# Performance work log

Measured on AMD Instinct MI355X. Metric: run time of the kernel, lower is better.

## Reference

```python
import jax, jax.numpy as jnp
import numpy as np

N, IN_CH, HID, HEADS, NCLS, E = 50000, 128, 32, 8, 16, 800000
NEG_SLOPE = 0.2  # PyG GATConv default negative_slope


def setup_inputs() -> dict:
    key = jax.random.key(0)
    ks = jax.random.split(key, 10)
    sc = lambda fan: 1.0 / np.sqrt(fan).astype(np.float32)
    x = jax.random.normal(ks[0], (N, IN_CH), jnp.float32)
    edge_index = jax.random.randint(ks[1], (2, E), 0, N, jnp.int32)
    W1 = jax.random.normal(ks[2], (IN_CH, HEADS * HID), jnp.float32) * sc(IN_CH)
    att_src1 = jax.random.normal(ks[3], (HEADS, HID), jnp.float32) * sc(HID)
    att_dst1 = jax.random.normal(ks[4], (HEADS, HID), jnp.float32) * sc(HID)
    b1 = jnp.zeros((HEADS * HID,), jnp.float32)
    W2 = jax.random.normal(ks[5], (HEADS * HID, NCLS), jnp.float32) * sc(HEADS * HID)
    att_src2 = jax.random.normal(ks[6], (1, NCLS), jnp.float32) * sc(NCLS)
    att_dst2 = jax.random.normal(ks[7], (1, NCLS), jnp.float32) * sc(NCLS)
    b2 = jnp.zeros((NCLS,), jnp.float32)
    return {"x": x, "edge_index": edge_index, "W1": W1, "att_src1": att_src1,
            "att_dst1": att_dst1, "b1": b1, "W2": W2, "att_src2": att_src2,
            "att_dst2": att_dst2, "b2": b2}


def _gat_layer(x, W, a_src, a_dst, src, dst, heads, ch):
    """PyG GATConv core: per-edge LeakyReLU attention, scatter-softmax over
    destination neighborhoods, scatter-add aggregation. Returns [N, heads, ch]."""
    n = x.shape[0]
    h = (x @ W).reshape(n, heads, ch)                      # [N,H,C]
    e_src = jnp.einsum('nhc,hc->nh', h, a_src)             # [N,H]
    e_dst = jnp.einsum('nhc,hc->nh', h, a_dst)             # [N,H]
    e = jax.nn.leaky_relu(e_src[src] + e_dst[dst], NEG_SLOPE)  # [Etot,H]
    # scatter-softmax grouped by destination node (self-loops ensure nonempty)
    m = jax.ops.segment_max(e, dst, num_segments=n)        # [N,H]
    p = jnp.exp(e - m[dst])
    denom = jax.ops.segment_sum(p, dst, num_segments=n)    # [N,H]
    alpha = p / denom[dst]                                 # [Etot,H]
    out = jax.ops.segment_sum(alpha[:, :, None] * h[src], dst, num_segments=n)
    return out                                             # [N,H,C]


def reference(x, edge_index, W1, att_src1, att_dst1, b1, W2, att_src2, att_dst2, b2):
    n = x.shape[0]
    loops = jnp.arange(n, dtype=edge_index.dtype)          # add_self_loops=True
    src = jnp.concatenate([edge_index[0], loops])
    dst = jnp.concatenate([edge_index[1], loops])
    # conv1: heads=8, concat=True
    h1 = _gat_layer(x, W1, att_src1, att_dst1, src, dst, HEADS, HID)
    h1 = h1.reshape(n, HEADS * HID) + b1
    h1 = jax.nn.elu(h1)  # dropout is identity in eval mode
    # conv2: heads=1, concat=False (mean over 1 head == that head)
    h2 = _gat_layer(h1, W2, att_src2, att_dst2, src, dst, 1, NCLS)
    return h2[:, 0, :] + b2
```

## Files before the change

kernel.cpp:

```cpp
#include <hip/hip_runtime.h>
#include <hip/hip_bf16.h>


#define IN_CH 128
#define HIDC  256
#define NCLS  16
#define NEG_SLOPE 0.2f

typedef short bf16x8 __attribute__((ext_vector_type(8)));
typedef float f32x4 __attribute__((ext_vector_type(4)));

__device__ __forceinline__ unsigned int f2bf(float f) {
    unsigned int u = __float_as_uint(f);
    return (u + 0x7fffu + ((u >> 16) & 1u)) >> 16;
}
__device__ __forceinline__ float bf_lo(unsigned int w) { return __uint_as_float(w << 16); }
__device__ __forceinline__ float bf_hi(unsigned int w) { return __uint_as_float(w & 0xffff0000u); }


__global__ void count_fill_kernel(const int* __restrict__ ei, int* __restrict__ counts,
                                  int E, int Etot,
                                  int* __restrict__ colB, int fill_n, int dummyB,
                                  unsigned short* __restrict__ Hb, float* __restrict__ ES1,
                                  float* __restrict__ H2, float* __restrict__ ES2,
                                  const float* __restrict__ W1,
                                  unsigned short* __restrict__ W1t, int N) {
    int i = blockIdx.x * blockDim.x + threadIdx.x;
    if (i < Etot) {
        int dst = (i < E) ? ei[E + i] : (i - E);
        atomicAdd(&counts[dst], 1);
    }
    if (i < fill_n) colB[i] = dummyB;
    if (i < IN_CH * HIDC) {
        int c = i >> 7, k = i & 127;
        W1t[i] = (unsigned short)f2bf(W1[k * HIDC + c]);
    }
    if (i < HIDC) Hb[(size_t)N * HIDC + i] = 0;
    if (i < NCLS) H2[(size_t)N * NCLS + i] = 0.f;
    if (i < 8) ES1[(size_t)N * 8 + i] = -3.0e38f;
    if (i == 0) ES2[N] = -3.0e38f;
}


__global__ __launch_bounds__(256) void scanA_kernel(const int* __restrict__ counts,
                                                    int* __restrict__ row_start,
                                                    int* __restrict__ bsums, int n) {
    __shared__ int wsum[4];
    int tid = threadIdx.x, lane = tid & 63, wid = tid >> 6;
    int i = blockIdx.x * 256 + tid;
    int v = (i < n) ? ((counts[i] + 3) & ~3) : 0;
    int x = v;
    #pragma unroll
    for (int off = 1; off < 64; off <<= 1) {
        int t = __shfl_up(x, off);
        if (lane >= off) x += t;
    }
    if (lane == 63) wsum[wid] = x;
    __syncthreads();
    if (tid < 4) {
        int w = wsum[tid];
        #pragma unroll
        for (int off = 1; off < 4; off <<= 1) {
            int t = __shfl_up(w, off);
            if (tid >= off) w += t;
        }
        wsum[tid] = w;
    }
    __syncthreads();
    int wex = wid ? wsum[wid - 1] : 0;
    if (i < n) row_start[i] = wex + (x - v);
    if (tid == 255) bsums[blockIdx.x] = wsum[3];
}

__global__ __launch_bounds__(256) void scanB_kernel(const int* __restrict__ bsums,
                                                    int* __restrict__ bofs,
                                                    int* __restrict__ row_start,
                                                    int nb, int n) {
    __shared__ int wsum[4];
    int tid = threadIdx.x, lane = tid & 63, wid = tid >> 6;
    int v = (tid < nb) ? bsums[tid] : 0;
    int x = v;
    #pragma unroll
    for (int off = 1; off < 64; off <<= 1) {
        int t = __shfl_up(x, off);
        if (lane >= off) x += t;
    }
    if (lane == 63) wsum[wid] = x;
    __syncthreads();
    if (tid < 4) {
        int w = wsum[tid];
        #pragma unroll
        for (int off = 1; off < 4; off <<= 1) {
            int t = __shfl_up(w, off);
            if (tid >= off) w += t;
        }
        wsum[tid] = w;
    }
    __syncthreads();
    int wex = wid ? wsum[wid - 1] : 0;
    if (tid < nb) bofs[tid] = wex + (x - v);
    if (tid == nb - 1) row_start[n] = wex + x;
}

__global__ __launch_bounds__(256) void scanC_kernel(int* __restrict__ row_start,
                                                    const int* __restrict__ bofs, int n) {
    int i = blockIdx.x * 256 + threadIdx.x;
    if (i < n) row_start[i] += bofs[blockIdx.x];
}

__global__ void scatter_kernel(const int* __restrict__ ei, const int* __restrict__ row_start,
                               int* __restrict__ cursor, int* __restrict__ colB,
                               int E, int Etot) {
    int e = blockIdx.x * blockDim.x + threadIdx.x;
    if (e >= Etot) return;
    int src, dst;
    if (e < E) { src = ei[e]; dst = ei[E + e]; }
    else       { src = e - E; dst = e - E; }
    int pos = row_start[dst] + atomicAdd(&cursor[dst], 1);
    colB[pos] = src * (HIDC * 2);
}


#define LDK 72

__global__ __launch_bounds__(256) void gemm1_mfma(const float* __restrict__ A,
                                                  const unsigned short* __restrict__ W1t,
                                                  const float* __restrict__ a_src,
                                                  const float* __restrict__ a_dst,
                                                  unsigned short* __restrict__ Hb,
                                                  float* __restrict__ ES,
                                                  float* __restrict__ ED, int M) {
    __shared__ unsigned short As[128 * LDK];
    __shared__ unsigned short Bs[128 * LDK];
    int tid = threadIdx.x;
    int row0 = blockIdx.x * 128, col0 = blockIdx.y * 128;
    int lane = tid & 63, wid = tid >> 6;
    int wr = wid >> 1, wc = wid & 1;
    int la = lane & 15, lg = lane >> 4;
    f32x4 acc[4][4] = {};

    int r = tid >> 1, hf = tid & 1;
    int gr = row0 + r;
    bool okA = gr < M;
    const float4* asrc = reinterpret_cast<const float4*>(A + (size_t)(okA ? gr : 0) * IN_CH) + hf * 8;
    const uint4*  bsrc = reinterpret_cast<const uint4*>(W1t + (size_t)(col0 + r) * IN_CH) + hf * 4;
    unsigned short* adst = &As[r * LDK + hf * 32];
    unsigned short* bdst = &Bs[r * LDK + hf * 32];

    #pragma unroll
    for (int kt = 0; kt < 2; ++kt) {
        #pragma unroll
        for (int it = 0; it < 8; ++it) {
            float4 v = okA ? asrc[it] : make_float4(0.f, 0.f, 0.f, 0.f);
            uint2 w;
            w.x = f2bf(v.x) | (f2bf(v.y) << 16);
            w.y = f2bf(v.z) | (f2bf(v.w) << 16);
            *reinterpret_cast<uint2*>(adst + it * 4) = w;
        }
        #pragma unroll
        for (int it = 0; it < 4; ++it) {
            uint4 v = bsrc[it];
            *reinterpret_cast<uint4*>(bdst + it * 8) = v;
        }
        asrc += 16;
        bsrc += 8;
        __syncthreads();
        #pragma unroll
        for (int k0 = 0; k0 < 64; k0 += 32) {
            bf16x8 af[4], bfr[4];
            #pragma unroll
            for (int m = 0; m < 4; ++m)
                af[m] = *reinterpret_cast<const bf16x8*>(&As[(wr * 64 + m * 16 + la) * LDK + k0 + lg * 8]);
            #pragma unroll
            for (int n2 = 0; n2 < 4; ++n2)
                bfr[n2] = *reinterpret_cast<const bf16x8*>(&Bs[(wc * 64 + n2 * 16 + la) * LDK + k0 + lg * 8]);
            #pragma unroll
            for (int m = 0; m < 4; ++m) {
                #pragma unroll
                for (int n2 = 0; n2 < 4; ++n2)
                    acc[m][n2] = __builtin_amdgcn_mfma_f32_16x16x32_bf16(af[m], bfr[n2], acc[m][n2], 0, 0, 0);
            }
        }
        __syncthreads();
    }

    #pragma unroll
    for (int m = 0; m < 4; ++m) {
        #pragma unroll
        for (int j = 0; j < 4; ++j) {
            int grow = row0 + wr * 64 + m * 16 + lg * 4 + j;
            if (grow < M) {
                int gcol = col0 + wc * 64 + la;
                #pragma unroll
                for (int n2 = 0; n2 < 4; ++n2)
                    Hb[(size_t)grow * HIDC + gcol + n2 * 16] = (unsigned short)f2bf(acc[m][n2][j]);
            }
        }
    }

    int h0 = (col0 + wc * 64) >> 5;
    float as00 = a_src[h0 * 32 + la],        as01 = a_src[h0 * 32 + 16 + la];
    float ad00 = a_dst[h0 * 32 + la],        ad01 = a_dst[h0 * 32 + 16 + la];
    float as10 = a_src[(h0 + 1) * 32 + la],  as11 = a_src[(h0 + 1) * 32 + 16 + la];
    float ad10 = a_dst[(h0 + 1) * 32 + la],  ad11 = a_dst[(h0 + 1) * 32 + 16 + la];
    #pragma unroll
    for (int m = 0; m < 4; ++m) {
        #pragma unroll
        for (int j = 0; j < 4; ++j) {
            float v0 = acc[m][0][j], v1 = acc[m][1][j];
            float v2 = acc[m][2][j], v3 = acc[m][3][j];
            float es0 = v0 * as00 + v1 * as01;
            float ed0 = v0 * ad00 + v1 * ad01;
            float es1 = v2 * as10 + v3 * as11;
            float ed1 = v2 * ad10 + v3 * ad11;
            #pragma unroll
            for (int off = 1; off < 16; off <<= 1) {
                es0 += __shfl_xor(es0, off);
                ed0 += __shfl_xor(ed0, off);
                es1 += __shfl_xor(es1, off);
                ed1 += __shfl_xor(ed1, off);
            }
            int grow = row0 + wr * 64 + m * 16 + lg * 4 + j;
            if (la == 0 && grow < M) {
                ES[grow * 8 + h0] = es0;
                ED[grow * 8 + h0] = ed0;
                ES[grow * 8 + h0 + 1] = es1;
                ED[grow * 8 + h0 + 1] = ed1;
            }
        }
    }
}


#define EDGE4(cbv)                                                              \
    {                                                                           \
        float e0 = *(const float*)(ESb + (((cbv).x >> 4) | hoff));              \
        float e1 = *(const float*)(ESb + (((cbv).y >> 4) | hoff));              \
        float e2 = *(const float*)(ESb + (((cbv).z >> 4) | hoff));              \
        float e3 = *(const float*)(ESb + (((cbv).w >> 4) | hoff));              \
        uint2 v0 = *(const uint2*)(Hbb + ((cbv).x + lane8));                    \
        uint2 v1 = *(const uint2*)(Hbb + ((cbv).y + lane8));                    \
        uint2 v2 = *(const uint2*)(Hbb + ((cbv).z + lane8));                    \
        uint2 v3 = *(const uint2*)(Hbb + ((cbv).w + lane8));                    \
        e0 += ed; e1 += ed; e2 += ed; e3 += ed;                                 \
        e0 = fmaxf(e0, NEG_SLOPE * e0);                                         \
        e1 = fmaxf(e1, NEG_SLOPE * e1);                                         \
        e2 = fmaxf(e2, NEG_SLOPE * e2);                                         \
        e3 = fmaxf(e3, NEG_SLOPE * e3);                                         \
        float p0 = __expf(e0), p1 = __expf(e1), p2 = __expf(e2), p3 = __expf(e3);\
        s += (p0 + p1) + (p2 + p3);                                             \
        acc.x = fmaf(p0, bf_lo(v0.x), acc.x);                                   \
        acc.y = fmaf(p0, bf_hi(v0.x), acc.y);                                   \
        acc.z = fmaf(p0, bf_lo(v0.y), acc.z);                                   \
        acc.w = fmaf(p0, bf_hi(v0.y), acc.w);                                   \
        acc.x = fmaf(p1, bf_lo(v1.x), acc.x);                                   \
        acc.y = fmaf(p1, bf_hi(v1.x), acc.y);                                   \
        acc.z = fmaf(p1, bf_lo(v1.y), acc.z);                                   \
        acc.w = fmaf(p1, bf_hi(v1.y), acc.w);                                   \
        acc.x = fmaf(p2, bf_lo(v2.x), acc.x);                                   \
        acc.y = fmaf(p2, bf_hi(v2.x), acc.y);                                   \
        acc.z = fmaf(p2, bf_lo(v2.y), acc.z);                                   \
        acc.w = fmaf(p2, bf_hi(v2.y), acc.w);                                   \
        acc.x = fmaf(p3, bf_lo(v3.x), acc.x);                                   \
        acc.y = fmaf(p3, bf_hi(v3.x), acc.y);                                   \
        acc.z = fmaf(p3, bf_lo(v3.y), acc.z);                                   \
        acc.w = fmaf(p3, bf_hi(v3.y), acc.w);                                   \
    }

__global__ __launch_bounds__(256) void agg1_kernel(const unsigned short* __restrict__ Hb,
                                                   const float* __restrict__ ES,
                                                   const float* __restrict__ ED,
                                                   const int* __restrict__ row_start,
                                                   const int* __restrict__ colB,
                                                   const float* __restrict__ b1,
                                                   float* __restrict__ h1, int N) {
    int n = blockIdx.x * 4 + (threadIdx.x >> 6);
    if (n >= N) return;
    int lane = threadIdx.x & 63;
    int h = lane >> 3;
    unsigned int hoff = h << 2;
    unsigned int lane8 = lane << 3;
    int s0 = row_start[n], s1 = row_start[n + 1];
    float ed = ED[n * 8 + h];
    const char* ESb = (const char*)ES;
    const char* Hbb = (const char*)Hb;

    float s = 0.f;
    float4 acc = make_float4(0.f, 0.f, 0.f, 0.f);

    int i = s0;
    for (; i + 7 < s1; i += 8) {
        uint4 cbA = *reinterpret_cast<const uint4*>(&colB[i]);
        uint4 cbB = *reinterpret_cast<const uint4*>(&colB[i + 4]);
        EDGE4(cbA);
        EDGE4(cbB);
    }
    if (i < s1) {
        uint4 cb = *reinterpret_cast<const uint4*>(&colB[i]);
        EDGE4(cb);
    }

    float inv = 1.0f / s;
    const float4 bv = *reinterpret_cast<const float4*>(&b1[lane * 4]);
    float4 o;
    o.x = acc.x * inv + bv.x;
    o.y = acc.y * inv + bv.y;
    o.z = acc.z * inv + bv.z;
    o.w = acc.w * inv + bv.w;
    o.x = o.x > 0.f ? o.x : expm1f(o.x);
    o.y = o.y > 0.f ? o.y : expm1f(o.y);
    o.z = o.z > 0.f ? o.z : expm1f(o.z);
    o.w = o.w > 0.f ? o.w : expm1f(o.w);
    *reinterpret_cast<float4*>(&h1[(size_t)n * HIDC + lane * 4]) = o;
}


__global__ __launch_bounds__(256) void gemm2_kernel(const float* __restrict__ X,
                                                    const float* __restrict__ W,
                                                    const float* __restrict__ a_src,
                                                    const float* __restrict__ a_dst,
                                                    float* __restrict__ Y,
                                                    float* __restrict__ ES2,
                                                    float* __restrict__ ED2, int N) {
    __shared__ float Ws[16][260];
    __shared__ float Xs[16][260];
    int tid = threadIdx.x;
    #pragma unroll
    for (int it = 0; it < 16; ++it) {
        int idx = tid + it * 256;
        int k = idx >> 4, c = idx & 15;
        Ws[c][k] = W[k * NCLS + c];
    }
    int row0 = blockIdx.x * 16;
    #pragma unroll
    for (int it = 0; it < 16; ++it) {
        int idx = tid + it * 256;
        int r = idx >> 8, k = idx & 255;
        int gr = row0 + r;
        Xs[r][k] = (gr < N) ? X[(size_t)gr * HIDC + k] : 0.f;
    }
    __syncthreads();
    int r = tid >> 4, c = tid & 15;
    float acc = 0.f;
    #pragma unroll 8
    for (int k = 0; k < 256; k += 4) {
        float4 xv = *reinterpret_cast<const float4*>(&Xs[r][k]);
        float4 wv = *reinterpret_cast<const float4*>(&Ws[c][k]);
        acc += xv.x * wv.x + xv.y * wv.y + xv.z * wv.z + xv.w * wv.w;
    }
    bool ok = (row0 + r) < N;
    if (ok) Y[(size_t)(row0 + r) * NCLS + c] = acc;
    float es = acc * a_src[c];
    float ed = acc * a_dst[c];
    #pragma unroll
    for (int off = 1; off < 16; off <<= 1) {
        es += __shfl_xor(es, off);
        ed += __shfl_xor(ed, off);
    }
    if (c == 0 && ok) {
        ES2[row0 + r] = es;
        ED2[row0 + r] = ed;
    }
}


__global__ __launch_bounds__(256) void agg2_kernel(const float* __restrict__ H2,
                                                   const float* __restrict__ ES,
                                                   const float* __restrict__ ED,
                                                   const int* __restrict__ row_start,
                                                   const int* __restrict__ colB,
                                                   const float* __restrict__ b2,
                                                   float* __restrict__ out, int N) {
    int g = blockIdx.x * 4 + (threadIdx.x >> 6);
    if (g >= N) return;
    int lane = threadIdx.x & 63;
    int ep = lane >> 4;
    unsigned int c4 = (lane & 15) << 2;
    int s0 = row_start[g], s1 = row_start[g + 1];
    float ed = ED[g];
    const char* ESb = (const char*)ES;
    const char* H2b = (const char*)H2;
    float s = 0.f, acc = 0.f;
    for (int i = s0 + ep; i < s1; i += 4) {
        unsigned int cb = (unsigned int)colB[i];
        float e = *(const float*)(ESb + (cb >> 7));
        float hv = *(const float*)(H2b + ((cb >> 3) | c4));
        e += ed;
        e = fmaxf(e, NEG_SLOPE * e);
        float p = __expf(e);
        s += p;
        acc = fmaf(p, hv, acc);
    }
    s += __shfl_xor(s, 16);
    s += __shfl_xor(s, 32);
    acc += __shfl_xor(acc, 16);
    acc += __shfl_xor(acc, 32);
    if ((lane & 48) == 0) out[(size_t)g * NCLS + (lane & 15)] = acc / s + b2[lane & 15];
}


extern "C" void kernel_launch(void* const* d_in, const int* in_sizes, int n_in,
                              void* d_out, int out_size, void* d_ws, size_t ws_size,
                              hipStream_t stream) {
    const float* x   = (const float*)d_in[0];
    const int*   ei  = (const int*)d_in[1];
    const float* W1  = (const float*)d_in[2];
    const float* as1 = (const float*)d_in[3];
    const float* ad1 = (const float*)d_in[4];
    const float* b1  = (const float*)d_in[5];
    const float* W2  = (const float*)d_in[6];
    const float* as2 = (const float*)d_in[7];
    const float* ad2 = (const float*)d_in[8];
    const float* b2  = (const float*)d_in[9];
    float* out = (float*)d_out;

    int N = in_sizes[0] / IN_CH;
    int E = in_sizes[1] / 2;
    int Etot = E + N;
    int fill_n = E + 4 * N;
    int nb = (N + 255) / 256;

    char* ws = (char*)d_ws;
    size_t off = 0;
    auto alloc = [&](size_t bytes) -> void* {
        void* p = ws + off;
        off += (bytes + 255) & ~(size_t)255;
        return p;
    };
    unsigned short* Hb  = (unsigned short*)alloc((size_t)(N + 1) * HIDC * 2);
    unsigned short* W1t = (unsigned short*)alloc((size_t)HIDC * IN_CH * 2);
    float* h1  = (float*)alloc((size_t)N * HIDC * 4);
    float* H2  = (float*)alloc((size_t)(N + 1) * NCLS * 4);
    float* ES1 = (float*)alloc((size_t)(N + 1) * 8 * 4);
    float* ED1 = (float*)alloc((size_t)N * 8 * 4);
    float* ES2 = (float*)alloc((size_t)(N + 1) * 4);
    float* ED2 = (float*)alloc((size_t)N * 4);
    int* counts = (int*)alloc((size_t)N * 2 * 4);
    int* cursor = counts + N;
    int* row_start = (int*)alloc((size_t)(N + 1) * 4);
    int* colB = (int*)alloc((size_t)fill_n * 4);
    int* bsums = (int*)alloc((size_t)256 * 4);
    int* bofs  = (int*)alloc((size_t)256 * 4);

    hipMemsetAsync(counts, 0, (size_t)N * 2 * 4, stream);

    int eb = (Etot + 255) / 256;
    count_fill_kernel<<<(fill_n + 255) / 256, 256, 0, stream>>>(
        ei, counts, E, Etot, colB, fill_n, N * HIDC * 2, Hb, ES1, H2, ES2, W1, W1t, N);
    scanA_kernel<<<nb, 256, 0, stream>>>(counts, row_start, bsums, N);
    scanB_kernel<<<1, 256, 0, stream>>>(bsums, bofs, row_start, nb, N);
    scanC_kernel<<<nb, 256, 0, stream>>>(row_start, bofs, N);
    scatter_kernel<<<eb, 256, 0, stream>>>(ei, row_start, cursor, colB, E, Etot);

    dim3 g1((N + 127) / 128, 2);
    gemm1_mfma<<<g1, 256, 0, stream>>>(x, W1t, as1, ad1, Hb, ES1, ED1, N);
    agg1_kernel<<<(N + 3) / 4, 256, 0, stream>>>(Hb, ES1, ED1, row_start, colB, b1, h1, N);
    gemm2_kernel<<<(N + 15) / 16, 256, 0, stream>>>(h1, W2, as2, ad2, H2, ES2, ED2, N);
    agg2_kernel<<<(N + 3) / 4, 256, 0, stream>>>(H2, ES2, ED2, row_start, colB, b2, out, N);
}
```

Before: 332.7 us.

## Fuse layer-2 projection into layer-1 aggregation and reuse count atomics for CSR ranks

Each wave in agg1 now computes the ELU'd hidden row, stages it in LDS and multiplies it by W2 (loaded into shared memory per block), emitting H2, ES2 and ED2 directly. This removes the gemm2 kernel and the 51 MB h1 round trip. The CSR build records each edge's atomic rank during counting, so the scatter no longer needs a second atomic pass over a cursor array. agg2 is also unrolled by two with split accumulators. The cost is a W2 load into LDS in every agg1 block of four nodes, extra LDS use that may lower occupancy, and an extra erank buffer write and read.

```diff
diff --git a/kernel.cpp b/kernel.cpp
--- a/kernel.cpp
+++ b/kernel.cpp
@@ -19,7 +19,7 @@
 
 
 __global__ void count_fill_kernel(const int* __restrict__ ei, int* __restrict__ counts,
-                                  int E, int Etot,
+                                  int* __restrict__ erank, int E, int Etot,
                                   int* __restrict__ colB, int fill_n, int dummyB,
                                   unsigned short* __restrict__ Hb, float* __restrict__ ES1,
                                   float* __restrict__ H2, float* __restrict__ ES2,
@@ -28,7 +28,7 @@
     int i = blockIdx.x * blockDim.x + threadIdx.x;
     if (i < Etot) {
         int dst = (i < E) ? ei[E + i] : (i - E);
-        atomicAdd(&counts[dst], 1);
+        erank[i] = atomicAdd(&counts[dst], 1);
     }
     if (i < fill_n) colB[i] = dummyB;
     if (i < IN_CH * HIDC) {
@@ -109,15 +109,14 @@
 }
 
 __global__ void scatter_kernel(const int* __restrict__ ei, const int* __restrict__ row_start,
-                               int* __restrict__ cursor, int* __restrict__ colB,
+                               const int* __restrict__ erank, int* __restrict__ colB,
                                int E, int Etot) {
     int e = blockIdx.x * blockDim.x + threadIdx.x;
     if (e >= Etot) return;
     int src, dst;
     if (e < E) { src = ei[e]; dst = ei[E + e]; }
     else       { src = e - E; dst = e - E; }
-    int pos = row_start[dst] + atomicAdd(&cursor[dst], 1);
-    colB[pos] = src * (HIDC * 2);
+    colB[row_start[dst] + erank[e]] = src * (HIDC * 2);
 }
 
 
@@ -273,10 +272,27 @@
                                                    const int* __restrict__ row_start,
                                                    const int* __restrict__ colB,
                                                    const float* __restrict__ b1,
-                                                   float* __restrict__ h1, int N) {
-    int n = blockIdx.x * 4 + (threadIdx.x >> 6);
+                                                   const float* __restrict__ W2,
+                                                   const float* __restrict__ as2,
+                                                   const float* __restrict__ ad2,
+                                                   float* __restrict__ H2,
+                                                   float* __restrict__ ES2,
+                                                   float* __restrict__ ED2, int N) {
+    __shared__ float W2t[16][260];
+    __shared__ float h1row[4][260];
+    int tid = threadIdx.x;
+    #pragma unroll
+    for (int it = 0; it < 16; ++it) {
+        int idx = tid + it * 256;
+        int c = idx & 15, k = idx >> 4;
+        W2t[c][k + (k >> 6)] = W2[idx];
+    }
+    __syncthreads();
+
+    int n = blockIdx.x * 4 + (tid >> 6);
     if (n >= N) return;
-    int lane = threadIdx.x & 63;
+    int lane = tid & 63;
+    int wv = tid >> 6;
     int h = lane >> 3;
     unsigned int hoff = h << 2;
     unsigned int lane8 = lane << 3;
@@ -311,55 +327,35 @@
     o.y = o.y > 0.f ? o.y : expm1f(o.y);
     o.z = o.z > 0.f ? o.z : expm1f(o.z);
     o.w = o.w > 0.f ? o.w : expm1f(o.w);
-    *reinterpret_cast<float4*>(&h1[(size_t)n * HIDC + lane * 4]) = o;
-}
-
-
-__global__ __launch_bounds__(256) void gemm2_kernel(const float* __restrict__ X,
-                                                    const float* __restrict__ W,
-                                                    const float* __restrict__ a_src,
-                                                    const float* __restrict__ a_dst,
-                                                    float* __restrict__ Y,
-                                                    float* __restrict__ ES2,
-                                                    float* __restrict__ ED2, int N) {
-    __shared__ float Ws[16][260];
-    __shared__ float Xs[16][260];
-    int tid = threadIdx.x;
-    #pragma unroll
-    for (int it = 0; it < 16; ++it) {
-        int idx = tid + it * 256;
-        int k = idx >> 4, c = idx & 15;
-        Ws[c][k] = W[k * NCLS + c];
-    }
-    int row0 = blockIdx.x * 16;
-    #pragma unroll
-    for (int it = 0; it < 16; ++it) {
-        int idx = tid + it * 256;
-        int r = idx >> 8, k = idx & 255;
-        int gr = row0 + r;
-        Xs[r][k] = (gr < N) ? X[(size_t)gr * HIDC + k] : 0.f;
-    }
-    __syncthreads();
-    int r = tid >> 4, c = tid & 15;
-    float acc = 0.f;
-    #pragma unroll 8
-    for (int k = 0; k < 256; k += 4) {
-        float4 xv = *reinterpret_cast<const float4*>(&Xs[r][k]);
-        float4 wv = *reinterpret_cast<const float4*>(&Ws[c][k]);
-        acc += xv.x * wv.x + xv.y * wv.y + xv.z * wv.z + xv.w * wv.w;
-    }
-    bool ok = (row0 + r) < N;
-    if (ok) Y[(size_t)(row0 + r) * NCLS + c] = acc;
-    float es = acc * a_src[c];
-    float ed = acc * a_dst[c];
-    #pragma unroll
-    for (int off = 1; off < 16; off <<= 1) {
-        es += __shfl_xor(es, off);
-        ed += __shfl_xor(ed, off);
-    }
-    if (c == 0 && ok) {
-        ES2[row0 + r] = es;
-        ED2[row0 + r] = ed;
+
+    {
+        float* hr = &h1row[wv][0];
+        int base = lane * 4 + (lane >> 4);
+        hr[base + 0] = o.x;
+        hr[base + 1] = o.y;
+        hr[base + 2] = o.z;
+        hr[base + 3] = o.w;
+        __builtin_amdgcn_wave_barrier();
+        int kg = lane >> 4, c = lane & 15;
+        const float* wcol = &W2t[c][kg * 65];
+        const float* hseg = &hr[kg * 65];
+        float p = 0.f;
+        #pragma unroll 16
+        for (int k = 0; k < 64; ++k) p = fmaf(hseg[k], wcol[k], p);
+        p += __shfl_xor(p, 16);
+        p += __shfl_xor(p, 32);
+        if (kg == 0) H2[(size_t)n * NCLS + c] = p;
+        float es = p * as2[c];
+        float edv = p * ad2[c];
+        #pragma unroll
+        for (int off = 1; off < 16; off <<= 1) {
+            es += __shfl_xor(es, off);
+            edv += __shfl_xor(edv, off);
+        }
+        if (lane == 0) {
+            ES2[n] = es;
+            ED2[n] = edv;
+        }
     }
 }
 
@@ -380,8 +376,24 @@
     float ed = ED[g];
     const char* ESb = (const char*)ES;
     const char* H2b = (const char*)H2;
-    float s = 0.f, acc = 0.f;
-    for (int i = s0 + ep; i < s1; i += 4) {
+    float s = 0.f, acc = 0.f, sB = 0.f, accB = 0.f;
+    int i = s0 + ep;
+    for (; i + 4 < s1; i += 8) {
+        unsigned int cb0 = (unsigned int)colB[i];
+        unsigned int cb1 = (unsigned int)colB[i + 4];
+        float e0 = *(const float*)(ESb + (cb0 >> 7));
+        float e1 = *(const float*)(ESb + (cb1 >> 7));
+        float hv0 = *(const float*)(H2b + ((cb0 >> 3) | c4));
+        float hv1 = *(const float*)(H2b + ((cb1 >> 3) | c4));
+        e0 += ed; e1 += ed;
+        e0 = fmaxf(e0, NEG_SLOPE * e0);
+        e1 = fmaxf(e1, NEG_SLOPE * e1);
+        float p0 = __expf(e0), p1 = __expf(e1);
+        s += p0; sB += p1;
+        acc = fmaf(p0, hv0, acc);
+        accB = fmaf(p1, hv1, accB);
+    }
+    if (i < s1) {
         unsigned int cb = (unsigned int)colB[i];
         float e = *(const float*)(ESb + (cb >> 7));
         float hv = *(const float*)(H2b + ((cb >> 3) | c4));
@@ -391,6 +403,7 @@
         s += p;
         acc = fmaf(p, hv, acc);
     }
+    s += sB; acc += accB;
     s += __shfl_xor(s, 16);
     s += __shfl_xor(s, 32);
     acc += __shfl_xor(acc, 16);
@@ -429,32 +442,31 @@
     };
     unsigned short* Hb  = (unsigned short*)alloc((size_t)(N + 1) * HIDC * 2);
     unsigned short* W1t = (unsigned short*)alloc((size_t)HIDC * IN_CH * 2);
-    float* h1  = (float*)alloc((size_t)N * HIDC * 4);
     float* H2  = (float*)alloc((size_t)(N + 1) * NCLS * 4);
     float* ES1 = (float*)alloc((size_t)(N + 1) * 8 * 4);
     float* ED1 = (float*)alloc((size_t)N * 8 * 4);
     float* ES2 = (float*)alloc((size_t)(N + 1) * 4);
     float* ED2 = (float*)alloc((size_t)N * 4);
-    int* counts = (int*)alloc((size_t)N * 2 * 4);
-    int* cursor = counts + N;
+    int* counts = (int*)alloc((size_t)N * 4);
+    int* erank  = (int*)alloc((size_t)Etot * 4);
     int* row_start = (int*)alloc((size_t)(N + 1) * 4);
     int* colB = (int*)alloc((size_t)fill_n * 4);
     int* bsums = (int*)alloc((size_t)256 * 4);
     int* bofs  = (int*)alloc((size_t)256 * 4);
 
-    hipMemsetAsync(counts, 0, (size_t)N * 2 * 4, stream);
+    hipMemsetAsync(counts, 0, (size_t)N * 4, stream);
 
     int eb = (Etot + 255) / 256;
     count_fill_kernel<<<(fill_n + 255) / 256, 256, 0, stream>>>(
-        ei, counts, E, Etot, colB, fill_n, N * HIDC * 2, Hb, ES1, H2, ES2, W1, W1t, N);
+        ei, counts, erank, E, Etot, colB, fill_n, N * HIDC * 2, Hb, ES1, H2, ES2, W1, W1t, N);
     scanA_kernel<<<nb, 256, 0, stream>>>(counts, row_start, bsums, N);
     scanB_kernel<<<1, 256, 0, stream>>>(bsums, bofs, row_start, nb, N);
     scanC_kernel<<<nb, 256, 0, stream>>>(row_start, bofs, N);
-    scatter_kernel<<<eb, 256, 0, stream>>>(ei, row_start, cursor, colB, E, Etot);
+    scatter_kernel<<<eb, 256, 0, stream>>>(ei, row_start, erank, colB, E, Etot);
 
     dim3 g1((N + 127) / 128, 2);
     gemm1_mfma<<<g1, 256, 0, stream>>>(x, W1t, as1, ad1, Hb, ES1, ED1, N);
-    agg1_kernel<<<(N + 3) / 4, 256, 0, stream>>>(Hb, ES1, ED1, row_start, colB, b1, h1, N);
-    gemm2_kernel<<<(N + 15) / 16, 256, 0, stream>>>(h1, W2, as2, ad2, H2, ES2, ED2, N);
+    agg1_kernel<<<(N + 3) / 4, 256, 0, stream>>>(Hb, ES1, ED1, row_start, colB, b1,
+                                                 W2, as2, ad2, H2, ES2, ED2, N);
     agg2_kernel<<<(N + 3) / 4, 256, 0, stream>>>(H2, ES2, ED2, row_start, colB, b2, out, N);
 }
```

After: 276.1 us. 1.21x faster.
